# Kernel optimization log

Hardware: AMD Instinct MI355X
Metric: run time of the kernel (lower is better)

Reference implementation:

```python
import jax, jax.numpy as jnp
import numpy as np

N, D, H, C = 50000, 128, 4, 16  # nodes, in_dim, heads, out per head
E, ED = 800000, 64              # edges, edge feature dim
NEG_SLOPE = 0.2


def setup_inputs() -> dict:
    key = jax.random.key(0)
    ks = jax.random.split(key, 10)
    x = jax.random.normal(ks[0], (N, D), dtype=jnp.float32)
    edge_index = jax.random.randint(ks[1], (2, E), 0, N, dtype=jnp.int64)
    edge_attr = jax.random.normal(ks[2], (E, ED), dtype=jnp.float32)
    s = 0.1
    W = jax.random.normal(ks[3], (H * C, D), dtype=jnp.float32) * s       # lin (no bias)
    W_edge = jax.random.normal(ks[4], (H * C, ED), dtype=jnp.float32) * s  # lin_edge (no bias)
    att_src = jax.random.normal(ks[5], (H, C), dtype=jnp.float32) * s
    att_dst = jax.random.normal(ks[6], (H, C), dtype=jnp.float32) * s
    att_edge = jax.random.normal(ks[7], (H, C), dtype=jnp.float32) * s
    bias = jnp.zeros((H * C,), dtype=jnp.float32)
    return dict(x=x, edge_index=edge_index, edge_attr=edge_attr, W=W,
                W_edge=W_edge, att_src=att_src, att_dst=att_dst,
                att_edge=att_edge, bias=bias)


def reference(x, edge_index, edge_attr, W, W_edge, att_src, att_dst, att_edge, bias):
    n = x.shape[0]
    src0, dst0 = edge_index[0], edge_index[1]

    # PyG GATConv default: add self-loops, self-loop edge_attr = per-dst mean of incoming edge_attr
    ones = jnp.ones((src0.shape[0],), dtype=edge_attr.dtype)
    cnt = jax.ops.segment_sum(ones, dst0, num_segments=n)                # [N]
    loop_attr = jax.ops.segment_sum(edge_attr, dst0, num_segments=n)
    loop_attr = loop_attr / jnp.maximum(cnt, 1.0)[:, None]               # [N, ED]
    ar = jnp.arange(n, dtype=src0.dtype)
    src = jnp.concatenate([src0, ar])
    dst = jnp.concatenate([dst0, ar])
    ea = jnp.concatenate([edge_attr, loop_attr], axis=0)                 # [E+N, ED]

    xh = (x @ W.T).reshape(n, H, C)                                      # [N, H, C]
    a_src = jnp.einsum('nhc,hc->nh', xh, att_src)                        # [N, H]
    a_dst = jnp.einsum('nhc,hc->nh', xh, att_dst)
    eh = (ea @ W_edge.T).reshape(-1, H, C)                               # [E+N, H, C]
    a_edge = jnp.einsum('ehc,hc->eh', eh, att_edge)                      # [E+N, H]

    alpha = a_src[src] + a_dst[dst] + a_edge                             # [E+N, H]
    alpha = jax.nn.leaky_relu(alpha, NEG_SLOPE)

    # softmax over edges grouped by destination node (PyG softmax)
    amax = jax.ops.segment_max(alpha, dst, num_segments=n)               # [N, H]
    alpha = jnp.exp(alpha - amax[dst])
    denom = jax.ops.segment_sum(alpha, dst, num_segments=n)
    alpha = alpha / (denom[dst] + 1e-16)

    # message = x_j * alpha, scatter-add to destination
    out = jax.ops.segment_sum(xh[src] * alpha[:, :, None], dst, num_segments=n)  # [N,H,C]
    return out.reshape(n, H * C) + bias
```

## Files before the change

### kernel.cpp

```cpp
#include <hip/hip_runtime.h>
#include <math.h>

#define N_NODES 50000
#define DIM     128
#define NHEAD   4
#define NCH     16
#define HC      64
#define NE      800000
#define EDIM    64
#define NEG     0.2f
#define MAXE    64

__device__ __forceinline__ float lrelu(float v) { return v > 0.f ? v : NEG * v; }

__global__ void k1_vedge(const float* __restrict__ W_edge, const float* __restrict__ att_edge,
                         float* __restrict__ v_edge) {
    int t = threadIdx.x;
    int h = t >> 6, d = t & 63;
    float acc = 0.f;
    #pragma unroll
    for (int c = 0; c < NCH; ++c)
        acc = fmaf(att_edge[h * NCH + c], W_edge[(h * NCH + c) * EDIM + d], acc);
    v_edge[h * 64 + d] = acc;
}

__global__ __launch_bounds__(256) void k2_xh(const float* __restrict__ x, const float* __restrict__ W,
                                             const float* __restrict__ att_src, const float* __restrict__ att_dst,
                                             float* __restrict__ xh, float* __restrict__ a_src,
                                             float* __restrict__ a_dst) {
    __shared__ float Wt[128 * 68];
    int t = threadIdx.x;
    for (int idx = t; idx < 64 * 128; idx += 256) {
        int col = idx >> 7, k = idx & 127;
        Wt[k * 68 + col] = W[idx];
    }
    __syncthreads();

    int h  = t & 3;
    int rp = t >> 2;
    int row0 = blockIdx.x * 128 + rp * 2;
    int r0 = min(row0, N_NODES - 1);
    int r1 = min(row0 + 1, N_NODES - 1);
    const float4* x0 = (const float4*)(x + (size_t)r0 * DIM);
    const float4* x1 = (const float4*)(x + (size_t)r1 * DIM);

    float acc0[16], acc1[16];
    #pragma unroll
    for (int c = 0; c < 16; ++c) { acc0[c] = 0.f; acc1[c] = 0.f; }

    for (int k4 = 0; k4 < 32; ++k4) {
        float4 xa = x0[k4];
        float4 xb = x1[k4];
        #pragma unroll
        for (int kk = 0; kk < 4; ++kk) {
            float va = (&xa.x)[kk];
            float vb = (&xb.x)[kk];
            const float* wr = &Wt[(k4 * 4 + kk) * 68 + h * 16];
            #pragma unroll
            for (int j = 0; j < 4; ++j) {
                float4 w = *(const float4*)(wr + 4 * j);
                acc0[4 * j + 0] = fmaf(va, w.x, acc0[4 * j + 0]);
                acc0[4 * j + 1] = fmaf(va, w.y, acc0[4 * j + 1]);
                acc0[4 * j + 2] = fmaf(va, w.z, acc0[4 * j + 2]);
                acc0[4 * j + 3] = fmaf(va, w.w, acc0[4 * j + 3]);
                acc1[4 * j + 0] = fmaf(vb, w.x, acc1[4 * j + 0]);
                acc1[4 * j + 1] = fmaf(vb, w.y, acc1[4 * j + 1]);
                acc1[4 * j + 2] = fmaf(vb, w.z, acc1[4 * j + 2]);
                acc1[4 * j + 3] = fmaf(vb, w.w, acc1[4 * j + 3]);
            }
        }
    }

    if (row0 < N_NODES) {
        float4* o = (float4*)(xh + (size_t)row0 * HC + h * 16);
        o[0] = make_float4(acc0[0], acc0[1], acc0[2], acc0[3]);
        o[1] = make_float4(acc0[4], acc0[5], acc0[6], acc0[7]);
        o[2] = make_float4(acc0[8], acc0[9], acc0[10], acc0[11]);
        o[3] = make_float4(acc0[12], acc0[13], acc0[14], acc0[15]);
        float ss = 0.f, sd = 0.f;
        #pragma unroll
        for (int c = 0; c < 16; ++c) {
            ss = fmaf(acc0[c], att_src[h * 16 + c], ss);
            sd = fmaf(acc0[c], att_dst[h * 16 + c], sd);
        }
        a_src[row0 * 4 + h] = ss;
        a_dst[row0 * 4 + h] = sd;
    }
    if (row0 + 1 < N_NODES) {
        float4* o = (float4*)(xh + (size_t)(row0 + 1) * HC + h * 16);
        o[0] = make_float4(acc1[0], acc1[1], acc1[2], acc1[3]);
        o[1] = make_float4(acc1[4], acc1[5], acc1[6], acc1[7]);
        o[2] = make_float4(acc1[8], acc1[9], acc1[10], acc1[11]);
        o[3] = make_float4(acc1[12], acc1[13], acc1[14], acc1[15]);
        float ss = 0.f, sd = 0.f;
        #pragma unroll
        for (int c = 0; c < 16; ++c) {
            ss = fmaf(acc1[c], att_src[h * 16 + c], ss);
            sd = fmaf(acc1[c], att_dst[h * 16 + c], sd);
        }
        a_src[(row0 + 1) * 4 + h] = ss;
        a_dst[(row0 + 1) * 4 + h] = sd;
    }
}

__global__ __launch_bounds__(256) void ka_deg(const int* __restrict__ ei, int* __restrict__ deg,
                                              int* __restrict__ rank) {
    int e = blockIdx.x * 256 + threadIdx.x;
    if (e >= NE) return;
    rank[e] = atomicAdd(deg + ei[NE + e], 1);
}

__global__ void k4a_scan(const int* __restrict__ deg, int* __restrict__ tmp, int* __restrict__ bsums) {
    int t = threadIdx.x;
    int i = blockIdx.x * 256 + t;
    int v = (i < N_NODES) ? deg[i] : 0;
    int lane = t & 63, w = t >> 6;
    int xv = v;
    #pragma unroll
    for (int o = 1; o < 64; o <<= 1) {
        int y = __shfl_up(xv, o);
        if (lane >= o) xv += y;
    }
    __shared__ int wtot[4];
    if (lane == 63) wtot[w] = xv;
    __syncthreads();
    int add = 0;
    #pragma unroll
    for (int j = 0; j < 4; ++j)
        if (j < w) add += wtot[j];
    xv += add;
    if (i < N_NODES) tmp[i] = xv;
    if (t == 255) bsums[blockIdx.x] = xv;
}

__global__ void k4b_scan(int* __restrict__ bsums, int nb) {
    int t = threadIdx.x;
    int v = (t < nb) ? bsums[t] : 0;
    int lane = t & 63, w = t >> 6;
    int xv = v;
    #pragma unroll
    for (int o = 1; o < 64; o <<= 1) {
        int y = __shfl_up(xv, o);
        if (lane >= o) xv += y;
    }
    __shared__ int wtot[4];
    if (lane == 63) wtot[w] = xv;
    __syncthreads();
    int add = 0;
    #pragma unroll
    for (int j = 0; j < 4; ++j)
        if (j < w) add += wtot[j];
    xv += add;
    if (t < nb) bsums[t] = xv - v;
}

__global__ void k4c_finish(const int* __restrict__ tmp, const int* __restrict__ bsums,
                           int* __restrict__ rowptr) {
    int i = blockIdx.x * 256 + threadIdx.x;
    if (i >= N_NODES) return;
    int incl = tmp[i] + bsums[i >> 8];
    rowptr[i + 1] = incl;
    if (i == 0) rowptr[0] = 0;
}

__global__ __launch_bounds__(256) void kp_compute(const float* __restrict__ edge_attr,
                                                  const float* __restrict__ v_edge,
                                                  float* __restrict__ p_tmp) {
    int lane = threadIdx.x & 63;
    int q = lane & 15;
    float4 w0 = *(const float4*)(v_edge + 0 * 64 + q * 4);
    float4 w1 = *(const float4*)(v_edge + 1 * 64 + q * 4);
    float4 w2 = *(const float4*)(v_edge + 2 * 64 + q * 4);
    float4 w3 = *(const float4*)(v_edge + 3 * 64 + q * 4);

    int wave   = (blockIdx.x * 256 + threadIdx.x) >> 6;
    int nwaves = gridDim.x * 4;
    for (int g = wave; g < NE / 4; g += nwaves) {
        float4 v = *(const float4*)(edge_attr + (size_t)g * 256 + lane * 4);
        float p0 = fmaf(v.x, w0.x, fmaf(v.y, w0.y, fmaf(v.z, w0.z, v.w * w0.w)));
        float p1 = fmaf(v.x, w1.x, fmaf(v.y, w1.y, fmaf(v.z, w1.z, v.w * w1.w)));
        float p2 = fmaf(v.x, w2.x, fmaf(v.y, w2.y, fmaf(v.z, w2.z, v.w * w2.w)));
        float p3 = fmaf(v.x, w3.x, fmaf(v.y, w3.y, fmaf(v.z, w3.z, v.w * w3.w)));
        #pragma unroll
        for (int m = 1; m < 16; m <<= 1) {
            p0 += __shfl_xor(p0, m);
            p1 += __shfl_xor(p1, m);
            p2 += __shfl_xor(p2, m);
            p3 += __shfl_xor(p3, m);
        }
        if (q == 0) {
            int e = g * 4 + (lane >> 4);
            *(float4*)(p_tmp + (size_t)e * 4) = make_float4(p0, p1, p2, p3);
        }
    }
}

__global__ __launch_bounds__(256) void kp_perm(const int* __restrict__ ei,
                                               const int* __restrict__ rank,
                                               const int* __restrict__ rowptr,
                                               int* __restrict__ perm) {
    int e = blockIdx.x * 256 + threadIdx.x;
    if (e >= NE) return;
    int dst = ei[NE + e];
    perm[rowptr[dst] + rank[e]] = e;
}

__global__ __launch_bounds__(256) void k6_agg(const int* __restrict__ rowptr,
                                              const int* __restrict__ perm,
                                              const int* __restrict__ ei,
                                              const float* __restrict__ p_tmp,
                                              const float* __restrict__ xh,
                                              const float* __restrict__ a_src,
                                              const float* __restrict__ a_dst,
                                              const float* __restrict__ bias,
                                              float* __restrict__ out) {
    __shared__ __align__(16) float s_w[4][MAXE][4];
    __shared__ int s_src[4][MAXE];
    int wid  = threadIdx.x >> 6;
    int lane = threadIdx.x & 63;
    int n = blockIdx.x * 4 + wid;
    int start = rowptr[n], end = rowptr[n + 1];
    int degn = end - start;
    int m = min(degn, MAXE);

    for (int i = lane; i < m; i += 64) {
        int e = perm[start + i];
        s_src[wid][i] = ei[e];
        *(float4*)&s_w[wid][i][0] = *(const float4*)(p_tmp + (size_t)e * 4);
    }
    __syncthreads();

    int h = lane & 3;
    float adh = a_dst[n * 4 + h];
    float sw = 0.f, sp = 0.f;
    for (int i = lane >> 2; i < m; i += 16) {
        int s   = s_src[wid][i];
        float p = s_w[wid][i][h];
        float w = __expf(lrelu(a_src[(size_t)s * 4 + h] + adh + p));
        s_w[wid][i][h] = w;
        sw += w;
        sp += p;
    }
    for (int i = MAXE + (lane >> 2); i < degn; i += 16) {
        int e = perm[start + i];
        int s = ei[e];
        float p = p_tmp[(size_t)e * 4 + h];
        sw += __expf(lrelu(a_src[(size_t)s * 4 + h] + adh + p));
        sp += p;
    }
    sw += __shfl_xor(sw, 4);  sp += __shfl_xor(sp, 4);
    sw += __shfl_xor(sw, 8);  sp += __shfl_xor(sp, 8);
    sw += __shfl_xor(sw, 16); sp += __shfl_xor(sp, 16);
    sw += __shfl_xor(sw, 32); sp += __shfl_xor(sp, 32);

    float al    = sp / fmaxf((float)degn, 1.f);
    float wself = __expf(lrelu(a_src[n * 4 + h] + adh + al));
    float denom = sw + wself + 1e-16f;
    __syncthreads();

    int h2 = lane >> 4;
    float d2   = __shfl(denom, h2);
    float ws2  = __shfl(wself, h2);
    float adh2 = __shfl(adh, h2);
    float acc = ws2 * xh[(size_t)n * HC + lane];

    int i = 0;
    for (; i + 4 <= m; i += 4) {
        int s0 = s_src[wid][i], s1 = s_src[wid][i + 1];
        int s2 = s_src[wid][i + 2], s3 = s_src[wid][i + 3];
        float w0 = s_w[wid][i][h2],     w1 = s_w[wid][i + 1][h2];
        float w2 = s_w[wid][i + 2][h2], w3 = s_w[wid][i + 3][h2];
        float x0 = xh[(size_t)s0 * HC + lane];
        float x1 = xh[(size_t)s1 * HC + lane];
        float x2 = xh[(size_t)s2 * HC + lane];
        float x3 = xh[(size_t)s3 * HC + lane];
        acc = fmaf(w0, x0, acc);
        acc = fmaf(w1, x1, acc);
        acc = fmaf(w2, x2, acc);
        acc = fmaf(w3, x3, acc);
    }
    for (; i < m; ++i) {
        int s = s_src[wid][i];
        acc = fmaf(s_w[wid][i][h2], xh[(size_t)s * HC + lane], acc);
    }
    for (int j = MAXE; j < degn; ++j) {
        int e = perm[start + j];
        int s = ei[e];
        float p = p_tmp[(size_t)e * 4 + h2];
        float w = __expf(lrelu(a_src[(size_t)s * 4 + h2] + adh2 + p));
        acc = fmaf(w, xh[(size_t)s * HC + lane], acc);
    }
    out[(size_t)n * HC + lane] = acc / d2 + bias[lane];
}

extern "C" void kernel_launch(void* const* d_in, const int* in_sizes, int n_in,
                              void* d_out, int out_size, void* d_ws, size_t ws_size,
                              hipStream_t stream) {
    const float* x         = (const float*)d_in[0];
    const int*   ei        = (const int*)d_in[1];
    const float* edge_attr = (const float*)d_in[2];
    const float* W         = (const float*)d_in[3];
    const float* W_edge    = (const float*)d_in[4];
    const float* att_src   = (const float*)d_in[5];
    const float* att_dst   = (const float*)d_in[6];
    const float* att_edge  = (const float*)d_in[7];
    const float* bias      = (const float*)d_in[8];
    float* out = (float*)d_out;

    char* ws = (char*)d_ws;
    size_t off = 0;
    float* v_edge    = (float*)(ws + off); off += 1024;
    float* xh        = (float*)(ws + off); off += (size_t)N_NODES * HC * 4;
    float* a_src     = (float*)(ws + off); off += (size_t)N_NODES * 4 * 4;
    float* a_dst     = (float*)(ws + off); off += (size_t)N_NODES * 4 * 4;
    int*   deg       = (int*)(ws + off);   off += (size_t)N_NODES * 4;
    int*   tmp       = (int*)(ws + off);   off += (size_t)N_NODES * 4;
    int*   bsums     = (int*)(ws + off);   off += 1024;
    int*   rowptr    = (int*)(ws + off);   off += (size_t)(N_NODES + 4) * 4;
    int*   rank      = (int*)(ws + off);   off += (size_t)NE * 4;
    int*   perm      = (int*)(ws + off);   off += (size_t)NE * 4;
    float* p_tmp     = (float*)(ws + off); off += (size_t)NE * 4 * 4;

    hipMemsetAsync(deg, 0, (size_t)N_NODES * 4, stream);

    k1_vedge<<<1, 256, 0, stream>>>(W_edge, att_edge, v_edge);
    k2_xh<<<(N_NODES + 127) / 128, 256, 0, stream>>>(x, W, att_src, att_dst, xh, a_src, a_dst);
    ka_deg<<<(NE + 255) / 256, 256, 0, stream>>>(ei, deg, rank);
    int nb = (N_NODES + 255) / 256;
    k4a_scan<<<nb, 256, 0, stream>>>(deg, tmp, bsums);
    k4b_scan<<<1, 256, 0, stream>>>(bsums, nb);
    k4c_finish<<<nb, 256, 0, stream>>>(tmp, bsums, rowptr);
    kp_compute<<<2048, 256, 0, stream>>>(edge_attr, v_edge, p_tmp);
    kp_perm<<<(NE + 255) / 256, 256, 0, stream>>>(ei, rank, rowptr, perm);
    k6_agg<<<N_NODES / 4, 256, 0, stream>>>(rowptr, perm, ei, p_tmp, xh,
                                            a_src, a_dst, bias, out);
}
```

Measured before the change: 449.2 us.

## Scatter edge sources and logits into CSR order; fold v_edge into kp_compute

Instead of building a permutation array and having the aggregation kernel do double-indirect loads (perm, then ei and p_tmp), the scatter kernel now writes source indices and per-edge attention logits directly into CSR-ordered arrays. The aggregation kernel can then read them contiguously. The tiny v_edge kernel is folded into each kp_compute block via shared memory, which removes one launch. The cost is extra scatter writes (a float4 per edge) and a redundant v_edge computation in every block.

```diff
diff --git a/kernel.cpp b/kernel.cpp
--- a/kernel.cpp
+++ b/kernel.cpp
@@ -12,17 +12,6 @@
 #define MAXE    64
 
 __device__ __forceinline__ float lrelu(float v) { return v > 0.f ? v : NEG * v; }
-
-__global__ void k1_vedge(const float* __restrict__ W_edge, const float* __restrict__ att_edge,
-                         float* __restrict__ v_edge) {
-    int t = threadIdx.x;
-    int h = t >> 6, d = t & 63;
-    float acc = 0.f;
-    #pragma unroll
-    for (int c = 0; c < NCH; ++c)
-        acc = fmaf(att_edge[h * NCH + c], W_edge[(h * NCH + c) * EDIM + d], acc);
-    v_edge[h * 64 + d] = acc;
-}
 
 __global__ __launch_bounds__(256) void k2_xh(const float* __restrict__ x, const float* __restrict__ W,
                                              const float* __restrict__ att_src, const float* __restrict__ att_dst,
@@ -164,16 +153,29 @@
 }
 
 __global__ __launch_bounds__(256) void kp_compute(const float* __restrict__ edge_attr,
-                                                  const float* __restrict__ v_edge,
+                                                  const float* __restrict__ W_edge,
+                                                  const float* __restrict__ att_edge,
                                                   float* __restrict__ p_tmp) {
-    int lane = threadIdx.x & 63;
+    __shared__ __align__(16) float sv[256];
+    int t = threadIdx.x;
+    {
+        int h = t >> 6, d = t & 63;
+        float acc = 0.f;
+        #pragma unroll
+        for (int c = 0; c < NCH; ++c)
+            acc = fmaf(att_edge[h * NCH + c], W_edge[(h * NCH + c) * EDIM + d], acc);
+        sv[h * 64 + d] = acc;
+    }
+    __syncthreads();
+
+    int lane = t & 63;
     int q = lane & 15;
-    float4 w0 = *(const float4*)(v_edge + 0 * 64 + q * 4);
-    float4 w1 = *(const float4*)(v_edge + 1 * 64 + q * 4);
-    float4 w2 = *(const float4*)(v_edge + 2 * 64 + q * 4);
-    float4 w3 = *(const float4*)(v_edge + 3 * 64 + q * 4);
-
-    int wave   = (blockIdx.x * 256 + threadIdx.x) >> 6;
+    float4 w0 = *(const float4*)(sv + 0 * 64 + q * 4);
+    float4 w1 = *(const float4*)(sv + 1 * 64 + q * 4);
+    float4 w2 = *(const float4*)(sv + 2 * 64 + q * 4);
+    float4 w3 = *(const float4*)(sv + 3 * 64 + q * 4);
+
+    int wave   = (blockIdx.x * 256 + t) >> 6;
     int nwaves = gridDim.x * 4;
     for (int g = wave; g < NE / 4; g += nwaves) {
         float4 v = *(const float4*)(edge_attr + (size_t)g * 256 + lane * 4);
@@ -195,20 +197,24 @@
     }
 }
 
-__global__ __launch_bounds__(256) void kp_perm(const int* __restrict__ ei,
-                                               const int* __restrict__ rank,
-                                               const int* __restrict__ rowptr,
-                                               int* __restrict__ perm) {
+__global__ __launch_bounds__(256) void kp_scatter(const int* __restrict__ ei,
+                                                  const int* __restrict__ rank,
+                                                  const int* __restrict__ rowptr,
+                                                  const float* __restrict__ p_tmp,
+                                                  int* __restrict__ csr_src,
+                                                  float* __restrict__ csr_p) {
     int e = blockIdx.x * 256 + threadIdx.x;
     if (e >= NE) return;
     int dst = ei[NE + e];
-    perm[rowptr[dst] + rank[e]] = e;
+    int pos = rowptr[dst] + rank[e];
+    float4 p = *(const float4*)(p_tmp + (size_t)e * 4);
+    csr_src[pos] = ei[e];
+    *(float4*)(csr_p + (size_t)pos * 4) = p;
 }
 
 __global__ __launch_bounds__(256) void k6_agg(const int* __restrict__ rowptr,
-                                              const int* __restrict__ perm,
-                                              const int* __restrict__ ei,
-                                              const float* __restrict__ p_tmp,
+                                              const int* __restrict__ csr_src,
+                                              const float* __restrict__ csr_p,
                                               const float* __restrict__ xh,
                                               const float* __restrict__ a_src,
                                               const float* __restrict__ a_dst,
@@ -224,9 +230,8 @@
     int m = min(degn, MAXE);
 
     for (int i = lane; i < m; i += 64) {
-        int e = perm[start + i];
-        s_src[wid][i] = ei[e];
-        *(float4*)&s_w[wid][i][0] = *(const float4*)(p_tmp + (size_t)e * 4);
+        s_src[wid][i] = csr_src[start + i];
+        *(float4*)&s_w[wid][i][0] = *(const float4*)(csr_p + (size_t)(start + i) * 4);
     }
     __syncthreads();
 
@@ -242,9 +247,8 @@
         sp += p;
     }
     for (int i = MAXE + (lane >> 2); i < degn; i += 16) {
-        int e = perm[start + i];
-        int s = ei[e];
-        float p = p_tmp[(size_t)e * 4 + h];
+        int s = csr_src[start + i];
+        float p = csr_p[(size_t)(start + i) * 4 + h];
         sw += __expf(lrelu(a_src[(size_t)s * 4 + h] + adh + p));
         sp += p;
     }
@@ -284,9 +288,8 @@
         acc = fmaf(s_w[wid][i][h2], xh[(size_t)s * HC + lane], acc);
     }
     for (int j = MAXE; j < degn; ++j) {
-        int e = perm[start + j];
-        int s = ei[e];
-        float p = p_tmp[(size_t)e * 4 + h2];
+        int s = csr_src[start + j];
+        float p = csr_p[(size_t)(start + j) * 4 + h2];
         float w = __expf(lrelu(a_src[(size_t)s * 4 + h2] + adh2 + p));
         acc = fmaf(w, xh[(size_t)s * HC + lane], acc);
     }
@@ -309,7 +312,6 @@
 
     char* ws = (char*)d_ws;
     size_t off = 0;
-    float* v_edge    = (float*)(ws + off); off += 1024;
     float* xh        = (float*)(ws + off); off += (size_t)N_NODES * HC * 4;
     float* a_src     = (float*)(ws + off); off += (size_t)N_NODES * 4 * 4;
     float* a_dst     = (float*)(ws + off); off += (size_t)N_NODES * 4 * 4;
@@ -318,20 +320,20 @@
     int*   bsums     = (int*)(ws + off);   off += 1024;
     int*   rowptr    = (int*)(ws + off);   off += (size_t)(N_NODES + 4) * 4;
     int*   rank      = (int*)(ws + off);   off += (size_t)NE * 4;
-    int*   perm      = (int*)(ws + off);   off += (size_t)NE * 4;
     float* p_tmp     = (float*)(ws + off); off += (size_t)NE * 4 * 4;
+    int*   csr_src   = (int*)(ws + off);   off += (size_t)NE * 4;
+    float* csr_p     = (float*)(ws + off); off += (size_t)NE * 4 * 4;
 
     hipMemsetAsync(deg, 0, (size_t)N_NODES * 4, stream);
 
-    k1_vedge<<<1, 256, 0, stream>>>(W_edge, att_edge, v_edge);
     k2_xh<<<(N_NODES + 127) / 128, 256, 0, stream>>>(x, W, att_src, att_dst, xh, a_src, a_dst);
     ka_deg<<<(NE + 255) / 256, 256, 0, stream>>>(ei, deg, rank);
     int nb = (N_NODES + 255) / 256;
     k4a_scan<<<nb, 256, 0, stream>>>(deg, tmp, bsums);
     k4b_scan<<<1, 256, 0, stream>>>(bsums, nb);
     k4c_finish<<<nb, 256, 0, stream>>>(tmp, bsums, rowptr);
-    kp_compute<<<2048, 256, 0, stream>>>(edge_attr, v_edge, p_tmp);
-    kp_perm<<<(NE + 255) / 256, 256, 0, stream>>>(ei, rank, rowptr, perm);
-    k6_agg<<<N_NODES / 4, 256, 0, stream>>>(rowptr, perm, ei, p_tmp, xh,
+    kp_compute<<<2048, 256, 0, stream>>>(edge_attr, W_edge, att_edge, p_tmp);
+    kp_scatter<<<(NE + 255) / 256, 256, 0, stream>>>(ei, rank, rowptr, p_tmp, csr_src, csr_p);
+    k6_agg<<<N_NODES / 4, 256, 0, stream>>>(rowptr, csr_src, csr_p, xh,
                                             a_src, a_dst, bias, out);
 }
```

Result: no change. 446.0 us (-0.7%).

## Fuse edge-attention projection into aggregation kernel, dropping p_tmp buffer

Applied to the files above, without the earlier changes.

Removes the separate v_edge and p_tmp kernels. Each aggregation block now recomputes v_edge in shared memory and computes per-edge attention logits directly from edge_attr, gathered by the permuted edge index. This avoids writing and re-reading the 12.8 MB p_tmp array and cuts two launches. In exchange, edge_attr rows are read in gathered (permuted) order rather than streamed, and every block recomputes the small v_edge product.

```diff
diff --git a/kernel.cpp b/kernel.cpp
--- a/kernel.cpp
+++ b/kernel.cpp
@@ -12,17 +12,6 @@
 #define MAXE    64
 
 __device__ __forceinline__ float lrelu(float v) { return v > 0.f ? v : NEG * v; }
-
-__global__ void k1_vedge(const float* __restrict__ W_edge, const float* __restrict__ att_edge,
-                         float* __restrict__ v_edge) {
-    int t = threadIdx.x;
-    int h = t >> 6, d = t & 63;
-    float acc = 0.f;
-    #pragma unroll
-    for (int c = 0; c < NCH; ++c)
-        acc = fmaf(att_edge[h * NCH + c], W_edge[(h * NCH + c) * EDIM + d], acc);
-    v_edge[h * 64 + d] = acc;
-}
 
 __global__ __launch_bounds__(256) void k2_xh(const float* __restrict__ x, const float* __restrict__ W,
                                              const float* __restrict__ att_src, const float* __restrict__ att_dst,
@@ -163,38 +152,6 @@
     if (i == 0) rowptr[0] = 0;
 }
 
-__global__ __launch_bounds__(256) void kp_compute(const float* __restrict__ edge_attr,
-                                                  const float* __restrict__ v_edge,
-                                                  float* __restrict__ p_tmp) {
-    int lane = threadIdx.x & 63;
-    int q = lane & 15;
-    float4 w0 = *(const float4*)(v_edge + 0 * 64 + q * 4);
-    float4 w1 = *(const float4*)(v_edge + 1 * 64 + q * 4);
-    float4 w2 = *(const float4*)(v_edge + 2 * 64 + q * 4);
-    float4 w3 = *(const float4*)(v_edge + 3 * 64 + q * 4);
-
-    int wave   = (blockIdx.x * 256 + threadIdx.x) >> 6;
-    int nwaves = gridDim.x * 4;
-    for (int g = wave; g < NE / 4; g += nwaves) {
-        float4 v = *(const float4*)(edge_attr + (size_t)g * 256 + lane * 4);
-        float p0 = fmaf(v.x, w0.x, fmaf(v.y, w0.y, fmaf(v.z, w0.z, v.w * w0.w)));
-        float p1 = fmaf(v.x, w1.x, fmaf(v.y, w1.y, fmaf(v.z, w1.z, v.w * w1.w)));
-        float p2 = fmaf(v.x, w2.x, fmaf(v.y, w2.y, fmaf(v.z, w2.z, v.w * w2.w)));
-        float p3 = fmaf(v.x, w3.x, fmaf(v.y, w3.y, fmaf(v.z, w3.z, v.w * w3.w)));
-        #pragma unroll
-        for (int m = 1; m < 16; m <<= 1) {
-            p0 += __shfl_xor(p0, m);
-            p1 += __shfl_xor(p1, m);
-            p2 += __shfl_xor(p2, m);
-            p3 += __shfl_xor(p3, m);
-        }
-        if (q == 0) {
-            int e = g * 4 + (lane >> 4);
-            *(float4*)(p_tmp + (size_t)e * 4) = make_float4(p0, p1, p2, p3);
-        }
-    }
-}
-
 __global__ __launch_bounds__(256) void kp_perm(const int* __restrict__ ei,
                                                const int* __restrict__ rank,
                                                const int* __restrict__ rowptr,
@@ -205,28 +162,68 @@
     perm[rowptr[dst] + rank[e]] = e;
 }
 
-__global__ __launch_bounds__(256) void k6_agg(const int* __restrict__ rowptr,
-                                              const int* __restrict__ perm,
-                                              const int* __restrict__ ei,
-                                              const float* __restrict__ p_tmp,
-                                              const float* __restrict__ xh,
-                                              const float* __restrict__ a_src,
-                                              const float* __restrict__ a_dst,
-                                              const float* __restrict__ bias,
-                                              float* __restrict__ out) {
+__global__ __launch_bounds__(256) void k6_mega(const int* __restrict__ rowptr,
+                                               const int* __restrict__ perm,
+                                               const int* __restrict__ ei,
+                                               const float* __restrict__ edge_attr,
+                                               const float* __restrict__ W_edge,
+                                               const float* __restrict__ att_edge,
+                                               const float* __restrict__ xh,
+                                               const float* __restrict__ a_src,
+                                               const float* __restrict__ a_dst,
+                                               const float* __restrict__ bias,
+                                               float* __restrict__ out) {
+    __shared__ __align__(16) float sv[256];
     __shared__ __align__(16) float s_w[4][MAXE][4];
     __shared__ int s_src[4][MAXE];
-    int wid  = threadIdx.x >> 6;
-    int lane = threadIdx.x & 63;
+    int t = threadIdx.x;
+    {
+        int h = t >> 6, d = t & 63;
+        float acc = 0.f;
+        #pragma unroll
+        for (int c = 0; c < NCH; ++c)
+            acc = fmaf(att_edge[h * NCH + c], W_edge[(h * NCH + c) * EDIM + d], acc);
+        sv[h * 64 + d] = acc;
+    }
+    __syncthreads();
+
+    int wid  = t >> 6;
+    int lane = t & 63;
     int n = blockIdx.x * 4 + wid;
     int start = rowptr[n], end = rowptr[n + 1];
     int degn = end - start;
     int m = min(degn, MAXE);
 
-    for (int i = lane; i < m; i += 64) {
-        int e = perm[start + i];
-        s_src[wid][i] = ei[e];
-        *(float4*)&s_w[wid][i][0] = *(const float4*)(p_tmp + (size_t)e * 4);
+    int sub = lane >> 4;
+    int q   = lane & 15;
+    float4 w0 = *(const float4*)(sv + 0 * 64 + q * 4);
+    float4 w1 = *(const float4*)(sv + 1 * 64 + q * 4);
+    float4 w2 = *(const float4*)(sv + 2 * 64 + q * 4);
+    float4 w3 = *(const float4*)(sv + 3 * 64 + q * 4);
+
+    for (int i0 = 0; i0 < m; i0 += 4) {
+        int i = i0 + sub;
+        float p0 = 0.f, p1 = 0.f, p2 = 0.f, p3 = 0.f;
+        int e = 0;
+        if (i < m) {
+            e = perm[start + i];
+            float4 v = *(const float4*)(edge_attr + (size_t)e * EDIM + q * 4);
+            p0 = fmaf(v.x, w0.x, fmaf(v.y, w0.y, fmaf(v.z, w0.z, v.w * w0.w)));
+            p1 = fmaf(v.x, w1.x, fmaf(v.y, w1.y, fmaf(v.z, w1.z, v.w * w1.w)));
+            p2 = fmaf(v.x, w2.x, fmaf(v.y, w2.y, fmaf(v.z, w2.z, v.w * w2.w)));
+            p3 = fmaf(v.x, w3.x, fmaf(v.y, w3.y, fmaf(v.z, w3.z, v.w * w3.w)));
+        }
+        #pragma unroll
+        for (int mm = 1; mm < 16; mm <<= 1) {
+            p0 += __shfl_xor(p0, mm);
+            p1 += __shfl_xor(p1, mm);
+            p2 += __shfl_xor(p2, mm);
+            p3 += __shfl_xor(p3, mm);
+        }
+        if (i < m && q == 0) {
+            s_src[wid][i] = ei[e];
+            *(float4*)&s_w[wid][i][0] = make_float4(p0, p1, p2, p3);
+        }
     }
     __syncthreads();
 
@@ -244,7 +241,10 @@
     for (int i = MAXE + (lane >> 2); i < degn; i += 16) {
         int e = perm[start + i];
         int s = ei[e];
-        float p = p_tmp[(size_t)e * 4 + h];
+        const float* ea = edge_attr + (size_t)e * EDIM;
+        const float* ve = sv + h * 64;
+        float p = 0.f;
+        for (int d = 0; d < EDIM; ++d) p = fmaf(ea[d], ve[d], p);
         sw += __expf(lrelu(a_src[(size_t)s * 4 + h] + adh + p));
         sp += p;
     }
@@ -268,16 +268,16 @@
     for (; i + 4 <= m; i += 4) {
         int s0 = s_src[wid][i], s1 = s_src[wid][i + 1];
         int s2 = s_src[wid][i + 2], s3 = s_src[wid][i + 3];
-        float w0 = s_w[wid][i][h2],     w1 = s_w[wid][i + 1][h2];
-        float w2 = s_w[wid][i + 2][h2], w3 = s_w[wid][i + 3][h2];
+        float w0w = s_w[wid][i][h2],     w1w = s_w[wid][i + 1][h2];
+        float w2w = s_w[wid][i + 2][h2], w3w = s_w[wid][i + 3][h2];
         float x0 = xh[(size_t)s0 * HC + lane];
         float x1 = xh[(size_t)s1 * HC + lane];
         float x2 = xh[(size_t)s2 * HC + lane];
         float x3 = xh[(size_t)s3 * HC + lane];
-        acc = fmaf(w0, x0, acc);
-        acc = fmaf(w1, x1, acc);
-        acc = fmaf(w2, x2, acc);
-        acc = fmaf(w3, x3, acc);
+        acc = fmaf(w0w, x0, acc);
+        acc = fmaf(w1w, x1, acc);
+        acc = fmaf(w2w, x2, acc);
+        acc = fmaf(w3w, x3, acc);
     }
     for (; i < m; ++i) {
         int s = s_src[wid][i];
@@ -286,7 +286,10 @@
     for (int j = MAXE; j < degn; ++j) {
         int e = perm[start + j];
         int s = ei[e];
-        float p = p_tmp[(size_t)e * 4 + h2];
+        const float* ea = edge_attr + (size_t)e * EDIM;
+        const float* ve = sv + h2 * 64;
+        float p = 0.f;
+        for (int d = 0; d < EDIM; ++d) p = fmaf(ea[d], ve[d], p);
         float w = __expf(lrelu(a_src[(size_t)s * 4 + h2] + adh2 + p));
         acc = fmaf(w, xh[(size_t)s * HC + lane], acc);
     }
@@ -309,7 +312,6 @@
 
     char* ws = (char*)d_ws;
     size_t off = 0;
-    float* v_edge    = (float*)(ws + off); off += 1024;
     float* xh        = (float*)(ws + off); off += (size_t)N_NODES * HC * 4;
     float* a_src     = (float*)(ws + off); off += (size_t)N_NODES * 4 * 4;
     float* a_dst     = (float*)(ws + off); off += (size_t)N_NODES * 4 * 4;
@@ -319,19 +321,16 @@
     int*   rowptr    = (int*)(ws + off);   off += (size_t)(N_NODES + 4) * 4;
     int*   rank      = (int*)(ws + off);   off += (size_t)NE * 4;
     int*   perm      = (int*)(ws + off);   off += (size_t)NE * 4;
-    float* p_tmp     = (float*)(ws + off); off += (size_t)NE * 4 * 4;
 
     hipMemsetAsync(deg, 0, (size_t)N_NODES * 4, stream);
 
-    k1_vedge<<<1, 256, 0, stream>>>(W_edge, att_edge, v_edge);
     k2_xh<<<(N_NODES + 127) / 128, 256, 0, stream>>>(x, W, att_src, att_dst, xh, a_src, a_dst);
     ka_deg<<<(NE + 255) / 256, 256, 0, stream>>>(ei, deg, rank);
     int nb = (N_NODES + 255) / 256;
     k4a_scan<<<nb, 256, 0, stream>>>(deg, tmp, bsums);
     k4b_scan<<<1, 256, 0, stream>>>(bsums, nb);
     k4c_finish<<<nb, 256, 0, stream>>>(tmp, bsums, rowptr);
-    kp_compute<<<2048, 256, 0, stream>>>(edge_attr, v_edge, p_tmp);
     kp_perm<<<(NE + 255) / 256, 256, 0, stream>>>(ei, rank, rowptr, perm);
-    k6_agg<<<N_NODES / 4, 256, 0, stream>>>(rowptr, perm, ei, p_tmp, xh,
-                                            a_src, a_dst, bias, out);
-}
+    k6_mega<<<N_NODES / 4, 256, 0, stream>>>(rowptr, perm, ei, edge_attr, W_edge, att_edge,
+                                             xh, a_src, a_dst, bias, out);
+}
```

Measured after the change: 534.8 us. 19.1% more time.
